# Performance work log

Measured on AMD Instinct MI355X. Metric: run time of the kernel, lower is better.

The kernel has to match this reference:

```python
import jax, jax.numpy as jnp
import numpy as np

VOL_LO = np.array([-40.0, -40.0, -1.0], np.float32)
VOL_HI = np.array([40.0, 40.0, 5.4], np.float32)
VOXEL = 0.4
GRID = (200, 200, 16)  # ((hi-lo)/voxel).int() as in __init__
NUM_CLASSES = 18
EMPTY_LABEL = 17
K = 10  # static per-gaussian tile: 6*sigma_max/VOXEL + 1 <= 10 since sigma <= 0.5
EPS = 1e-6
N_GAUSS = 8192


def quat_to_rotmat(q):
    # wxyz quaternion -> rotation matrix (normalized, as in 3DGS)
    q = q / jnp.linalg.norm(q, axis=-1, keepdims=True)
    w, x, y, z = q[..., 0], q[..., 1], q[..., 2], q[..., 3]
    R = jnp.stack([
        1 - 2 * (y * y + z * z), 2 * (x * y - w * z), 2 * (x * z + w * y),
        2 * (x * y + w * z), 1 - 2 * (x * x + z * z), 2 * (y * z - w * x),
        2 * (x * z - w * y), 2 * (y * z + w * x), 1 - 2 * (x * x + y * y),
    ], axis=-1)
    return R.reshape(q.shape[:-1] + (3, 3))


def _grid_coords():
    H, W, D = GRID
    ii, jj, kk = jnp.meshgrid(jnp.arange(H), jnp.arange(W), jnp.arange(D), indexing='ij')
    g = jnp.stack([ii, jj, kk], axis=-1).astype(jnp.float32) + 0.5  # voxel centers
    return g * VOXEL + jnp.asarray(VOL_LO)


def setup_inputs() -> dict:
    key = jax.random.key(0)
    k1, k2, k3, k4, k5 = jax.random.split(key, 5)
    lo = jnp.asarray(VOL_LO)
    hi = jnp.asarray(VOL_HI)
    means3d = jax.random.uniform(k1, (N_GAUSS, 3)) * (hi - lo) + lo
    opacities = jax.random.uniform(k2, (N_GAUSS, 1))
    features = jax.random.normal(k3, (N_GAUSS, NUM_CLASSES - 1))
    scales = jax.random.uniform(k4, (N_GAUSS, 3)) * 0.4 + 0.1  # sigma in [0.1, 0.5]
    rotations = jax.random.normal(k5, (N_GAUSS, 4))
    empty_scalar = jnp.full((1,), 10.0, jnp.float32)
    return {"means3d": means3d, "opacities": opacities, "features": features,
            "scales": scales, "rotations": rotations, "empty_scalar": empty_scalar}


def reference(means3d, opacities, features, scales, rotations, empty_scalar):
    H, W, D = GRID
    lo = jnp.asarray(VOL_LO)
    hi = jnp.asarray(VOL_HI)
    dims = jnp.array(GRID, jnp.int32)

    # covariances = (R diag(s)) (R diag(s))^T
    R = quat_to_rotmat(rotations)                 # [N,3,3]
    Lm = R * scales[:, None, :]
    cov = Lm @ jnp.swapaxes(Lm, -1, -2)           # [N,3,3]
    cov_inv = jnp.linalg.inv(cov)
    sig = jnp.sqrt(jnp.diagonal(cov, axis1=-2, axis2=-1))  # [N,3]

    # clamped 3-sigma bounds + skip test (strict, matching torch)
    b_lo = jnp.clip(means3d - 3.0 * sig, lo, hi)
    b_hi = jnp.clip(means3d + 3.0 * sig, lo, hi)
    valid = (((b_lo > lo) | (b_hi > lo)) & ((b_lo < hi) | (b_hi < hi))).all(-1)  # [N]
    i_lo = ((b_lo - lo) / VOXEL).astype(jnp.int32)
    i_hi = ((b_hi - lo) / VOXEL).astype(jnp.int32)

    # static KxKxK tile per gaussian, masked to the inclusive [i_lo, i_hi] slice
    o = jnp.arange(K, dtype=jnp.int32)
    oi, oj, ok = jnp.meshgrid(o, o, o, indexing='ij')
    offs = jnp.stack([oi, oj, ok], -1).reshape(-1, 3)          # [K3,3]
    vox = i_lo[:, None, :] + offs[None]                        # [N,K3,3]
    mask = (vox <= i_hi[:, None, :]).all(-1) & (vox < dims).all(-1) & valid[:, None]

    coords = (vox.astype(jnp.float32) + 0.5) * VOXEL + lo      # voxel centers
    diff = coords - means3d[:, None, :]                        # [N,K3,3]
    maha = jnp.einsum('nki,nij,nkj->nk', diff, cov_inv, diff)  # [N,K3]
    dens = jnp.where(mask, opacities * jnp.exp(-0.5 * maha), 0.0)

    flat = jnp.where(mask, vox[..., 0] * (W * D) + vox[..., 1] * D + vox[..., 2], 0)

    feat18 = jnp.concatenate([features, jnp.zeros_like(features[:, :1])], -1)  # [N,18]
    gd = jnp.zeros((H * W * D,), jnp.float32).at[flat.reshape(-1)].add(dens.reshape(-1))
    gf = jnp.zeros((H * W * D, NUM_CLASSES), jnp.float32).at[flat.reshape(-1)].add(
        (dens[..., None] * feat18[:, None, :]).reshape(-1, NUM_CLASSES))

    # appended 'empty' gaussian spans the full grid -> splat densely
    gc = _grid_coords()                                        # [H,W,D,3]
    e_mean = (lo + hi) / 2.0
    e_range = hi - lo
    e_inv = jnp.diag(1.0 / (e_range ** 2))
    de = gc - e_mean
    maha_e = jnp.einsum('hwdi,ij,hwdj->hwd', de, e_inv, de)
    dens_e = jnp.exp(-0.5 * maha_e)                            # empty opacity = 1
    e_feat = jnp.zeros((NUM_CLASSES,), jnp.float32).at[EMPTY_LABEL].add(empty_scalar[0])

    grid_density = gd.reshape(H, W, D) + dens_e
    grid_feats = gf.reshape(H, W, D, NUM_CLASSES) + dens_e[..., None] * e_feat
    grid_feats = grid_feats / jnp.maximum(grid_density[..., None], EPS)
    return grid_density[..., None], grid_feats
```

## Files before the change

### kernel.cpp

```cpp
#include <hip/hip_runtime.h>

namespace {
constexpr int GH = 200, GW = 200, GD = 16;
constexpr int NV = GH * GW * GD;
constexpr int NCLS = 18;
constexpr int NF = 17;
constexpr int NG = 8192;
constexpr int KMAX = 10;
constexpr float VOX = 0.4f;
constexpr float LO0 = -40.f, LO1 = -40.f, LO2 = -1.f;
constexpr float HI0 = 40.f, HI1 = 40.f, HI2 = 5.4f;
constexpr float EPSV = 1e-6f;

constexpr int TILE_XY = 4;
constexpr int NTX = GH / TILE_XY;
constexpr int NTY = GW / TILE_XY;
constexpr int NT = NTX * NTY;
constexpr int REC_DW = 32;
constexpr int CAP = 1024;
}

__global__ __launch_bounds__(256) void gv_bin(
    const float* __restrict__ means,
    const float* __restrict__ opac,
    const float* __restrict__ feats,
    const float* __restrict__ scales,
    const float* __restrict__ rots,
    int4* __restrict__ boxes,
    float* __restrict__ recs,
    int* __restrict__ counts,
    int* __restrict__ lists)
{
    const int g = blockIdx.x * blockDim.x + threadIdx.x;
    if (g >= NG) return;

    const float mx = means[g * 3 + 0];
    const float my = means[g * 3 + 1];
    const float mz = means[g * 3 + 2];
    const float sx = scales[g * 3 + 0];
    const float sy = scales[g * 3 + 1];
    const float sz = scales[g * 3 + 2];
    float qw = rots[g * 4 + 0];
    float qx = rots[g * 4 + 1];
    float qy = rots[g * 4 + 2];
    float qz = rots[g * 4 + 3];

    const float qn = rsqrtf(qw * qw + qx * qx + qy * qy + qz * qz);
    qw *= qn; qx *= qn; qy *= qn; qz *= qn;
    const float r00 = 1.f - 2.f * (qy * qy + qz * qz);
    const float r01 = 2.f * (qx * qy - qw * qz);
    const float r02 = 2.f * (qx * qz + qw * qy);
    const float r10 = 2.f * (qx * qy + qw * qz);
    const float r11 = 1.f - 2.f * (qx * qx + qz * qz);
    const float r12 = 2.f * (qy * qz - qw * qx);
    const float r20 = 2.f * (qx * qz - qw * qy);
    const float r21 = 2.f * (qy * qz + qw * qx);
    const float r22 = 1.f - 2.f * (qx * qx + qy * qy);

    const float s0 = sx * sx, s1 = sy * sy, s2 = sz * sz;
    const float c00 = r00 * r00 * s0 + r01 * r01 * s1 + r02 * r02 * s2;
    const float c11 = r10 * r10 * s0 + r11 * r11 * s1 + r12 * r12 * s2;
    const float c22 = r20 * r20 * s0 + r21 * r21 * s1 + r22 * r22 * s2;
    const float i0 = 1.f / s0, i1 = 1.f / s1, i2 = 1.f / s2;
    const float a00 = r00 * r00 * i0 + r01 * r01 * i1 + r02 * r02 * i2;
    const float a01 = r00 * r10 * i0 + r01 * r11 * i1 + r02 * r12 * i2;
    const float a02 = r00 * r20 * i0 + r01 * r21 * i1 + r02 * r22 * i2;
    const float a11 = r10 * r10 * i0 + r11 * r11 * i1 + r12 * r12 * i2;
    const float a12 = r10 * r20 * i0 + r11 * r21 * i1 + r12 * r22 * i2;
    const float a22 = r20 * r20 * i0 + r21 * r21 * i1 + r22 * r22 * i2;

    const float m3[3] = { mx, my, mz };
    const float sg[3] = { sqrtf(c00), sqrtf(c11), sqrtf(c22) };
    const float lo3[3] = { LO0, LO1, LO2 };
    const float hi3[3] = { HI0, HI1, HI2 };
    const int dims[3] = { GH, GW, GD };

    int il[3], sp[3];
    bool valid = true;
#pragma unroll
    for (int ax = 0; ax < 3; ++ax) {
        const float bl = fminf(fmaxf(m3[ax] - 3.f * sg[ax], lo3[ax]), hi3[ax]);
        const float bh = fminf(fmaxf(m3[ax] + 3.f * sg[ax], lo3[ax]), hi3[ax]);
        valid = valid &&
                (((bl > lo3[ax]) || (bh > lo3[ax])) && ((bl < hi3[ax]) || (bh < hi3[ax])));
        const int a = (int)((bl - lo3[ax]) / VOX);
        const int b = (int)((bh - lo3[ax]) / VOX);
        int s = b - a + 1;
        s = min(s, KMAX);
        s = min(s, dims[ax] - a);
        s = max(s, 0);
        il[ax] = a;
        sp[ax] = s;
    }

    boxes[g] = make_int4(il[0], il[1], il[2], sp[0] | (sp[1] << 8) | (sp[2] << 16));

    float* R = recs + (size_t)g * REC_DW;
    R[0] = mx; R[1] = my; R[2] = mz; R[3] = opac[g];
    R[4] = a00; R[5] = a01; R[6] = a02; R[7] = a11; R[8] = a12; R[9] = a22;
#pragma unroll
    for (int c = 0; c < NF; ++c) R[10 + c] = feats[g * NF + c];

    if (!valid || sp[0] <= 0 || sp[1] <= 0 || sp[2] <= 0) return;

    const int tx0 = il[0] / TILE_XY;
    const int tx1 = (il[0] + sp[0] - 1) / TILE_XY;
    const int ty0 = il[1] / TILE_XY;
    const int ty1 = (il[1] + sp[1] - 1) / TILE_XY;
    for (int tx = tx0; tx <= tx1; ++tx)
        for (int ty = ty0; ty <= ty1; ++ty) {
            const int tile = tx * NTY + ty;
            const int idx = atomicAdd(counts + tile, 1);
            if (idx < CAP) lists[(size_t)tile * CAP + idx] = g;
        }
}

__global__ __launch_bounds__(64) void gv_gather(
    const int4* __restrict__ boxes,
    const float* __restrict__ recs,
    const int* __restrict__ counts,
    const int* __restrict__ lists,
    const float* __restrict__ empty_scalar,
    float* __restrict__ out)
{
    const int tile = blockIdx.x;
    const int tx = tile / NTY;
    const int ty = tile - tx * NTY;

    const int lane = threadIdx.x;
    const int lx = lane >> 4;
    const int ly = (lane >> 2) & 3;
    const int vz0 = (lane & 3) << 2;

    const int vx = tx * TILE_XY + lx;
    const int vy = ty * TILE_XY + ly;
    const float cx = ((float)vx + 0.5f) * VOX + LO0;
    const float cy = ((float)vy + 0.5f) * VOX + LO1;

    const int n = min(counts[tile], CAP);
    const int* __restrict__ lst = lists + (size_t)tile * CAP;

    float accd[4] = { 0.f, 0.f, 0.f, 0.f };
    float accf[4][NF];
#pragma unroll
    for (int j = 0; j < 4; ++j)
#pragma unroll
        for (int c = 0; c < NF; ++c) accf[j][c] = 0.f;

    int4 b1 = make_int4(0, 0, 0, 0);
    float P1[27];
#pragma unroll
    for (int u = 0; u < 27; ++u) P1[u] = 0.f;
    if (n > 0) {
        const int g = __builtin_amdgcn_readfirstlane(lst[0]);
        b1 = boxes[g];
        const float* R = recs + (size_t)g * REC_DW;
#pragma unroll
        for (int u = 0; u < 27; ++u) P1[u] = R[u];
    }

    for (int i = 0; i < n; ++i) {
        const int4 b0 = b1;
        float P0[27];
#pragma unroll
        for (int u = 0; u < 27; ++u) P0[u] = P1[u];

        if (i + 1 < n) {
            const int g = __builtin_amdgcn_readfirstlane(lst[i + 1]);
            b1 = boxes[g];
            const float* R = recs + (size_t)g * REC_DW;
#pragma unroll
            for (int u = 0; u < 27; ++u) P1[u] = R[u];
        }

        const bool inxy =
            ((unsigned)(vx - b0.x) < (unsigned)(b0.w & 255)) &
            ((unsigned)(vy - b0.y) < (unsigned)((b0.w >> 8) & 255));
        const unsigned spz = (unsigned)((b0.w >> 16) & 255);

        const float dx = cx - P0[0];
        const float dy = cy - P0[1];
        const float q0 = P0[4] * dx * dx + P0[7] * dy * dy + 2.f * P0[5] * dx * dy;
        const float q1 = 2.f * (P0[6] * dx + P0[8] * dy);

#pragma unroll
        for (int j = 0; j < 4; ++j) {
            const float cz = ((float)(vz0 + j) + 0.5f) * VOX + LO2;
            const float dz = cz - P0[2];
            const float maha = q0 + dz * (q1 + P0[9] * dz);
            const bool in = inxy & ((unsigned)(vz0 + j - b0.z) < spz);
            const float dens = P0[3] * __expf(-0.5f * maha);
            if (in) {
                accd[j] += dens;
#pragma unroll
                for (int c = 0; c < NF; ++c) accf[j][c] += dens * P0[10 + c];
            }
        }
    }

    const float es = empty_scalar[0];
    const float ex = (cx - 0.5f * (LO0 + HI0)) / (HI0 - LO0);
    const float ey = (cy - 0.5f * (LO1 + HI1)) / (HI1 - LO1);
    const float exy = ex * ex + ey * ey;

    float dsv[4], dev[4];
#pragma unroll
    for (int j = 0; j < 4; ++j) {
        const float cz = ((float)(vz0 + j) + 0.5f) * VOX + LO2;
        const float ez = (cz - 0.5f * (LO2 + HI2)) / (HI2 - LO2);
        dev[j] = __expf(-0.5f * (exy + ez * ez));
        dsv[j] = accd[j] + dev[j];
    }

    const int vbase = (vx * GW + vy) * GD + vz0;
    *(float4*)(out + vbase) = make_float4(dsv[0], dsv[1], dsv[2], dsv[3]);

#pragma unroll
    for (int j = 0; j < 4; ++j) {
        const float inv = 1.f / fmaxf(dsv[j], EPSV);
        float vals[NCLS];
#pragma unroll
        for (int c = 0; c < NF; ++c) vals[c] = accf[j][c] * inv;
        vals[NF] = dev[j] * es * inv;
        float2* of2 = (float2*)(out + NV + (size_t)(vbase + j) * NCLS);
#pragma unroll
        for (int p = 0; p < NCLS / 2; ++p)
            of2[p] = make_float2(vals[2 * p], vals[2 * p + 1]);
    }
}

extern "C" void kernel_launch(void* const* d_in, const int* in_sizes, int n_in,
                              void* d_out, int out_size, void* d_ws, size_t ws_size,
                              hipStream_t stream) {
    const float* means  = (const float*)d_in[0];
    const float* opac   = (const float*)d_in[1];
    const float* feats  = (const float*)d_in[2];
    const float* scales = (const float*)d_in[3];
    const float* rots   = (const float*)d_in[4];
    const float* esc    = (const float*)d_in[5];

    int4*  boxes  = (int4*)d_ws;
    float* recs   = (float*)(boxes + NG);
    int*   counts = (int*)(recs + (size_t)NG * REC_DW);
    int*   lists  = counts + ((NT + 63) & ~63);

    hipMemsetAsync(counts, 0, sizeof(int) * ((NT + 63) & ~63), stream);

    gv_bin<<<NG / 256, 256, 0, stream>>>(means, opac, feats, scales, rots,
                                         boxes, recs, counts, lists);
    gv_gather<<<NT, 64, 0, stream>>>(boxes, recs, counts, lists, esc, (float*)d_out);
}
```

Measured before the change: 108.3 us.

## Stage gaussian records through double-buffered LDS chunks with packed box and prescaled conic

The box metadata is folded into the 32-dword per-gaussian record. The conic coefficients are prescaled by -0.5*log2(e) so the inner loop can use exp2f directly. The gather kernel no longer does per-gaussian scalar global loads with register prefetch. Instead it cooperatively loads chunks of 32 records into double-buffered shared memory with float4 vector loads, overlapping the next chunk's global load with compute on the current one. This adds a block barrier per chunk and reads from LDS in the inner loop, which should cut global-load latency exposure.

```diff
diff --git a/kernel.cpp b/kernel.cpp
--- a/kernel.cpp
+++ b/kernel.cpp
@@ -17,7 +17,11 @@
 constexpr int NTY = GW / TILE_XY;
 constexpr int NT = NTX * NTY;
 constexpr int REC_DW = 32;
+constexpr int REC_V4 = REC_DW / 4;
 constexpr int CAP = 1024;
+constexpr int CH = 32;
+
+constexpr float NHL2E = -0.72134752044448170368f;
 }
 
 __global__ __launch_bounds__(256) void gv_bin(
@@ -26,7 +30,6 @@
     const float* __restrict__ feats,
     const float* __restrict__ scales,
     const float* __restrict__ rots,
-    int4* __restrict__ boxes,
     float* __restrict__ recs,
     int* __restrict__ counts,
     int* __restrict__ lists)
@@ -93,15 +96,22 @@
         sp[ax] = s;
     }
 
-    boxes[g] = make_int4(il[0], il[1], il[2], sp[0] | (sp[1] << 8) | (sp[2] << 16));
-
-    float* R = recs + (size_t)g * REC_DW;
-    R[0] = mx; R[1] = my; R[2] = mz; R[3] = opac[g];
-    R[4] = a00; R[5] = a01; R[6] = a02; R[7] = a11; R[8] = a12; R[9] = a22;
-#pragma unroll
-    for (int c = 0; c < NF; ++c) R[10 + c] = feats[g * NF + c];
-
-    if (!valid || sp[0] <= 0 || sp[1] <= 0 || sp[2] <= 0) return;
+    const bool live = valid && sp[0] > 0 && sp[1] > 0 && sp[2] > 0;
+    const int pack = live ? (sp[0] | (sp[1] << 8) | (sp[2] << 16)) : 0;
+
+    float4* R4 = (float4*)(recs + (size_t)g * REC_DW);
+    const float* F = feats + (size_t)g * NF;
+    R4[0] = make_float4(mx, my, mz, opac[g]);
+    R4[1] = make_float4(NHL2E * a00, NHL2E * a11, NHL2E * a22, 2.f * NHL2E * a01);
+    R4[2] = make_float4(2.f * NHL2E * a02, 2.f * NHL2E * a12, F[0], F[1]);
+    R4[3] = make_float4(F[2], F[3], F[4], F[5]);
+    R4[4] = make_float4(F[6], F[7], F[8], F[9]);
+    R4[5] = make_float4(F[10], F[11], F[12], F[13]);
+    R4[6] = make_float4(F[14], F[15], F[16], __int_as_float(il[0]));
+    R4[7] = make_float4(__int_as_float(il[1]), __int_as_float(il[2]),
+                        __int_as_float(pack), 0.f);
+
+    if (!live) return;
 
     const int tx0 = il[0] / TILE_XY;
     const int tx1 = (il[0] + sp[0] - 1) / TILE_XY;
@@ -116,13 +126,14 @@
 }
 
 __global__ __launch_bounds__(64) void gv_gather(
-    const int4* __restrict__ boxes,
     const float* __restrict__ recs,
     const int* __restrict__ counts,
     const int* __restrict__ lists,
     const float* __restrict__ empty_scalar,
     float* __restrict__ out)
 {
+    __shared__ float4 s_rec[2][CH * REC_V4];
+
     const int tile = blockIdx.x;
     const int tx = tile / NTY;
     const int ty = tile - tx * NTY;
@@ -147,55 +158,81 @@
 #pragma unroll
         for (int c = 0; c < NF; ++c) accf[j][c] = 0.f;
 
-    int4 b1 = make_int4(0, 0, 0, 0);
-    float P1[27];
-#pragma unroll
-    for (int u = 0; u < 27; ++u) P1[u] = 0.f;
-    if (n > 0) {
-        const int g = __builtin_amdgcn_readfirstlane(lst[0]);
-        b1 = boxes[g];
-        const float* R = recs + (size_t)g * REC_DW;
-#pragma unroll
-        for (int u = 0; u < 27; ++u) P1[u] = R[u];
-    }
-
-    for (int i = 0; i < n; ++i) {
-        const int4 b0 = b1;
-        float P0[27];
-#pragma unroll
-        for (int u = 0; u < 27; ++u) P0[u] = P1[u];
-
-        if (i + 1 < n) {
-            const int g = __builtin_amdgcn_readfirstlane(lst[i + 1]);
-            b1 = boxes[g];
-            const float* R = recs + (size_t)g * REC_DW;
-#pragma unroll
-            for (int u = 0; u < 27; ++u) P1[u] = R[u];
-        }
-
-        const bool inxy =
-            ((unsigned)(vx - b0.x) < (unsigned)(b0.w & 255)) &
-            ((unsigned)(vy - b0.y) < (unsigned)((b0.w >> 8) & 255));
-        const unsigned spz = (unsigned)((b0.w >> 16) & 255);
-
-        const float dx = cx - P0[0];
-        const float dy = cy - P0[1];
-        const float q0 = P0[4] * dx * dx + P0[7] * dy * dy + 2.f * P0[5] * dx * dy;
-        const float q1 = 2.f * (P0[6] * dx + P0[8] * dy);
-
-#pragma unroll
-        for (int j = 0; j < 4; ++j) {
-            const float cz = ((float)(vz0 + j) + 0.5f) * VOX + LO2;
-            const float dz = cz - P0[2];
-            const float maha = q0 + dz * (q1 + P0[9] * dz);
-            const bool in = inxy & ((unsigned)(vz0 + j - b0.z) < spz);
-            const float dens = P0[3] * __expf(-0.5f * maha);
-            if (in) {
-                accd[j] += dens;
-#pragma unroll
-                for (int c = 0; c < NF; ++c) accf[j][c] += dens * P0[10 + c];
+    const int e_ld = lane >> 1;
+    const int q_ld = lane & 1;
+    float4 r0, r1, r2, r3;
+
+    const int nchunk = (n + CH - 1) / CH;
+    int buf = 0;
+
+    if (nchunk > 0) {
+        const int idx = e_ld;
+        if (idx < n) {
+            const float4* src = (const float4*)recs + (size_t)lst[idx] * REC_V4 + q_ld * 4;
+            r0 = src[0]; r1 = src[1]; r2 = src[2]; r3 = src[3];
+            float4* dst = &s_rec[0][e_ld * REC_V4 + q_ld * 4];
+            dst[0] = r0; dst[1] = r1; dst[2] = r2; dst[3] = r3;
+        }
+    }
+    __syncthreads();
+
+    for (int c = 0; c < nchunk; ++c) {
+        const int nidx = (c + 1) * CH + e_ld;
+        const bool nact = (c + 1 < nchunk) && (nidx < n);
+        if (nact) {
+            const float4* src = (const float4*)recs + (size_t)lst[nidx] * REC_V4 + q_ld * 4;
+            r0 = src[0]; r1 = src[1]; r2 = src[2]; r3 = src[3];
+        }
+
+        const int m = min(CH, n - c * CH);
+        for (int e = 0; e < m; ++e) {
+            const float4* E = &s_rec[buf][e * REC_V4];
+            const float4 e0 = E[0], e1 = E[1], e2 = E[2], e3 = E[3];
+            const float4 e4 = E[4], e5 = E[5], e6 = E[6], e7 = E[7];
+
+            const int il0 = __float_as_int(e6.w);
+            const int il1 = __float_as_int(e7.x);
+            const int il2 = __float_as_int(e7.y);
+            const int pk  = __float_as_int(e7.z);
+
+            const bool inxy =
+                ((unsigned)(vx - il0) < (unsigned)(pk & 255)) &
+                ((unsigned)(vy - il1) < (unsigned)((pk >> 8) & 255));
+            const unsigned spz = (unsigned)((pk >> 16) & 255);
+
+            const float dx = cx - e0.x;
+            const float dy = cy - e0.y;
+            const float q0 = e1.x * dx * dx + e1.y * dy * dy + e1.w * dx * dy;
+            const float q1 = e2.x * dx + e2.y * dy;
+            const float A22 = e1.z;
+            const float op = e0.w, mzv = e0.z;
+
+            const float f[NF] = { e2.z, e2.w, e3.x, e3.y, e3.z, e3.w,
+                                  e4.x, e4.y, e4.z, e4.w,
+                                  e5.x, e5.y, e5.z, e5.w,
+                                  e6.x, e6.y, e6.z };
+
+#pragma unroll
+            for (int j = 0; j < 4; ++j) {
+                const float cz = ((float)(vz0 + j) + 0.5f) * VOX + LO2;
+                const float dz = cz - mzv;
+                const float ee = q0 + dz * (q1 + A22 * dz);
+                const bool in = inxy & ((unsigned)(vz0 + j - il2) < spz);
+                const float dens = op * exp2f(ee);
+                if (in) {
+                    accd[j] += dens;
+#pragma unroll
+                    for (int cc = 0; cc < NF; ++cc) accf[j][cc] += dens * f[cc];
+                }
             }
         }
+
+        if (nact) {
+            float4* dst = &s_rec[buf ^ 1][e_ld * REC_V4 + q_ld * 4];
+            dst[0] = r0; dst[1] = r1; dst[2] = r2; dst[3] = r3;
+        }
+        __syncthreads();
+        buf ^= 1;
     }
 
     const float es = empty_scalar[0];
@@ -239,14 +276,13 @@
     const float* rots   = (const float*)d_in[4];
     const float* esc    = (const float*)d_in[5];
 
-    int4*  boxes  = (int4*)d_ws;
-    float* recs   = (float*)(boxes + NG);
+    float* recs   = (float*)d_ws;
     int*   counts = (int*)(recs + (size_t)NG * REC_DW);
     int*   lists  = counts + ((NT + 63) & ~63);
 
     hipMemsetAsync(counts, 0, sizeof(int) * ((NT + 63) & ~63), stream);
 
     gv_bin<<<NG / 256, 256, 0, stream>>>(means, opac, feats, scales, rots,
-                                         boxes, recs, counts, lists);
-    gv_gather<<<NT, 64, 0, stream>>>(boxes, recs, counts, lists, esc, (float*)d_out);
-}
+                                         recs, counts, lists);
+    gv_gather<<<NT, 64, 0, stream>>>(recs, counts, lists, esc, (float*)d_out);
+}
```

After: 105.4 us. 2.7% less time.
